# Kernel optimization log

Hardware: AMD Instinct MI355X
Metric: run time of the kernel (lower is better)

Reference implementation:

```python
import jax, jax.numpy as jnp
import numpy as np

CHANNELS = 96


def make_sharpen_kernel(channels: int) -> jnp.ndarray:
    # (C_out, C_in, 3, 3), block-diagonal: per-channel 3x3 sharpen stencil
    k = jnp.full((3, 3), -0.1, dtype=jnp.float32).at[1, 1].set(1.8)
    eye = jnp.eye(channels, dtype=jnp.float32)  # (C, C)
    return eye[:, :, None, None] * k[None, None, :, :]


def setup_inputs() -> dict:
    key = jax.random.key(0)
    x = jax.random.normal(key, (16, CHANNELS, 256, 256), dtype=jnp.float32)
    kernel = make_sharpen_kernel(CHANNELS)
    return {"x": x, "kernel": kernel}


def reference(x, kernel):
    # Faithful to F.conv2d(x, kernel, stride=1, padding=1) with the dense
    # (block-diagonal) kernel the torch module constructs.
    return jax.lax.conv_general_dilated(
        x, kernel,
        window_strides=(1, 1),
        padding=((1, 1), (1, 1)),
        dimension_numbers=("NCHW", "OIHW", "NCHW"),
    )
```

## Files before the change

### kernel.cpp

```cpp
#include <hip/hip_runtime.h>

#define CHN 96
#define IMG_H 256
#define IMG_W 256
#define STRIP 16
#define WPB 4
#define NXCD 8

typedef float vfloat4 __attribute__((ext_vector_type(4)));

__device__ __forceinline__ vfloat4 ldrow(const float* xp, int yy, int col) {
    if (yy < IMG_H)
        return __builtin_nontemporal_load(
            (const vfloat4*)(xp + (size_t)yy * IMG_W + col));
    return (vfloat4){0.f, 0.f, 0.f, 0.f};
}

__device__ __forceinline__ vfloat4 hsum3(vfloat4 v, int lane) {
    float l = __shfl_up(v.w, 1);
    float r = __shfl_down(v.x, 1);
    if (lane == 0)  l = 0.f;
    if (lane == 63) r = 0.f;
    float t1 = v.x + v.y;
    float t2 = v.z + v.w;
    vfloat4 h;
    h.x = l   + t1;
    h.y = t1  + v.z;
    h.z = v.y + t2;
    h.w = t2  + r;
    return h;
}

__global__ __launch_bounds__(WPB * 64)
void sharpen3x3_flat(const float* __restrict__ x,
                     const float* __restrict__ kern,
                     float* __restrict__ out)
{
    const int lane = threadIdx.x & 63;
    const int wave = threadIdx.x >> 6;

    const int chunk = gridDim.x / NXCD;
    const int bid   = (blockIdx.x % NXCD) * chunk + blockIdx.x / NXCD;

    const int strip_id = bid * WPB + wave;
    const int spp      = IMG_H / STRIP;
    const int plane    = strip_id / spp;
    const int sy       = (strip_id % spp) * STRIP;
    const int c        = plane % CHN;

    const float* kw = kern + ((size_t)c * CHN + c) * 9;
    const float wn = kw[0];
    const float wd = kw[4] - wn;

    const float* xp = x   + (size_t)plane * IMG_H * IMG_W;
    float*       op = out + (size_t)plane * IMG_H * IMG_W;
    const int col = 4 * lane;

    vfloat4 buf[STRIP];
    #pragma unroll
    for (int j = 0; j < STRIP; ++j) buf[j] = ldrow(xp, sy + 1 + j, col);

    vfloat4 vtop = (sy == 0) ? (vfloat4){0.f, 0.f, 0.f, 0.f}
                             : *(const vfloat4*)(xp + (size_t)(sy - 1) * IMG_W + col);
    vfloat4 v0   = *(const vfloat4*)(xp + (size_t)sy * IMG_W + col);

    vfloat4 hprev = hsum3(vtop, lane);
    if (sy == 0) hprev = (vfloat4){0.f, 0.f, 0.f, 0.f};
    vfloat4 hcur = hsum3(v0, lane);
    vfloat4 ccur = v0;

    #pragma unroll
    for (int j = 0; j < STRIP; ++j) {
        vfloat4 hn = hsum3(buf[j], lane);
        vfloat4 s  = hprev + hcur + hn;
        vfloat4 o  = s * wn + ccur * wd;
        __builtin_nontemporal_store(
            o, (vfloat4*)(op + (size_t)(sy + j) * IMG_W + col));
        hprev = hcur;
        hcur  = hn;
        ccur  = buf[j];
    }
}

extern "C" void kernel_launch(void* const* d_in, const int* in_sizes, int n_in,
                              void* d_out, int out_size, void* d_ws, size_t ws_size,
                              hipStream_t stream) {
    const float* x    = (const float*)d_in[0];
    const float* kern = (const float*)d_in[1];
    float* out        = (float*)d_out;

    const int n_strips = 16 * CHN * (IMG_H / STRIP);
    const int grid     = n_strips / WPB;

    hipLaunchKernelGGL(sharpen3x3_flat, dim3(grid), dim3(WPB * 64),
                       0, stream, x, kern, out);
}
```

Baseline: 150.1 us.

## Double-buffer row loads in groups of eight with longer strips, drop XCD remap

Each wave now processes a 32-row strip instead of 16. It ping-pongs between two 8-row register buffers so the next group's loads are issued while the current group is computed and stored. The XCD-aware block index remapping is removed, and fewer halo rows are re-read per strip. The trade-offs are fewer waves in flight for latency hiding, and a possible change in L2 locality across XCDs.

```diff
diff --git a/kernel.cpp b/kernel.cpp
--- a/kernel.cpp
+++ b/kernel.cpp
@@ -3,9 +3,9 @@
 #define CHN 96
 #define IMG_H 256
 #define IMG_W 256
-#define STRIP 16
+#define STRIP 32
 #define WPB 4
-#define NXCD 8
+#define GRP 8
 
 typedef float vfloat4 __attribute__((ext_vector_type(4)));
 
@@ -14,6 +14,12 @@
         return __builtin_nontemporal_load(
             (const vfloat4*)(xp + (size_t)yy * IMG_W + col));
     return (vfloat4){0.f, 0.f, 0.f, 0.f};
+}
+
+__device__ __forceinline__ void ldgroup(vfloat4* buf, const float* xp,
+                                        int y0, int col) {
+    #pragma unroll
+    for (int j = 0; j < GRP; ++j) buf[j] = ldrow(xp, y0 + j, col);
 }
 
 __device__ __forceinline__ vfloat4 hsum3(vfloat4 v, int lane) {
@@ -31,18 +37,33 @@
     return h;
 }
 
+__device__ __forceinline__ void compute_group(const vfloat4* buf,
+                                              vfloat4& hprev, vfloat4& hcur,
+                                              vfloat4& ccur,
+                                              float wn, float wd,
+                                              float* op, int y, int col, int lane) {
+    #pragma unroll
+    for (int j = 0; j < GRP; ++j) {
+        vfloat4 hn = hsum3(buf[j], lane);
+        vfloat4 s  = hprev + hcur + hn;
+        vfloat4 o  = s * wn + ccur * wd;
+        __builtin_nontemporal_store(
+            o, (vfloat4*)(op + (size_t)(y + j) * IMG_W + col));
+        hprev = hcur;
+        hcur  = hn;
+        ccur  = buf[j];
+    }
+}
+
 __global__ __launch_bounds__(WPB * 64)
-void sharpen3x3_flat(const float* __restrict__ x,
-                     const float* __restrict__ kern,
-                     float* __restrict__ out)
+void sharpen3x3_pp2(const float* __restrict__ x,
+                    const float* __restrict__ kern,
+                    float* __restrict__ out)
 {
     const int lane = threadIdx.x & 63;
     const int wave = threadIdx.x >> 6;
 
-    const int chunk = gridDim.x / NXCD;
-    const int bid   = (blockIdx.x % NXCD) * chunk + blockIdx.x / NXCD;
-
-    const int strip_id = bid * WPB + wave;
+    const int strip_id = blockIdx.x * WPB + wave;
     const int spp      = IMG_H / STRIP;
     const int plane    = strip_id / spp;
     const int sy       = (strip_id % spp) * STRIP;
@@ -56,30 +77,28 @@
     float*       op = out + (size_t)plane * IMG_H * IMG_W;
     const int col = 4 * lane;
 
-    vfloat4 buf[STRIP];
-    #pragma unroll
-    for (int j = 0; j < STRIP; ++j) buf[j] = ldrow(xp, sy + 1 + j, col);
-
     vfloat4 vtop = (sy == 0) ? (vfloat4){0.f, 0.f, 0.f, 0.f}
                              : *(const vfloat4*)(xp + (size_t)(sy - 1) * IMG_W + col);
     vfloat4 v0   = *(const vfloat4*)(xp + (size_t)sy * IMG_W + col);
+
+    vfloat4 A[GRP], B[GRP];
+    ldgroup(A, xp, sy + 1, col);
 
     vfloat4 hprev = hsum3(vtop, lane);
     if (sy == 0) hprev = (vfloat4){0.f, 0.f, 0.f, 0.f};
     vfloat4 hcur = hsum3(v0, lane);
     vfloat4 ccur = v0;
 
-    #pragma unroll
-    for (int j = 0; j < STRIP; ++j) {
-        vfloat4 hn = hsum3(buf[j], lane);
-        vfloat4 s  = hprev + hcur + hn;
-        vfloat4 o  = s * wn + ccur * wd;
-        __builtin_nontemporal_store(
-            o, (vfloat4*)(op + (size_t)(sy + j) * IMG_W + col));
-        hprev = hcur;
-        hcur  = hn;
-        ccur  = buf[j];
-    }
+    ldgroup(B, xp, sy + GRP + 1, col);
+    compute_group(A, hprev, hcur, ccur, wn, wd, op, sy, col, lane);
+
+    ldgroup(A, xp, sy + 2 * GRP + 1, col);
+    compute_group(B, hprev, hcur, ccur, wn, wd, op, sy + GRP, col, lane);
+
+    ldgroup(B, xp, sy + 3 * GRP + 1, col);
+    compute_group(A, hprev, hcur, ccur, wn, wd, op, sy + 2 * GRP, col, lane);
+
+    compute_group(B, hprev, hcur, ccur, wn, wd, op, sy + 3 * GRP, col, lane);
 }
 
 extern "C" void kernel_launch(void* const* d_in, const int* in_sizes, int n_in,
@@ -92,6 +111,6 @@
     const int n_strips = 16 * CHN * (IMG_H / STRIP);
     const int grid     = n_strips / WPB;
 
-    hipLaunchKernelGGL(sharpen3x3_flat, dim3(grid), dim3(WPB * 64),
+    hipLaunchKernelGGL(sharpen3x3_pp2, dim3(grid), dim3(WPB * 64),
                        0, stream, x, kern, out);
 }
```

New measurement: 144.2 us. -3.9%, faster.
